# Kernel optimization log

Measured on AMD Instinct MI355X. Metric: run time of the kernel, lower is better.

## Reference

```python
import jax, jax.numpy as jnp
import numpy as np
import itertools

B, T, C, H = 2, 512, 768, 12
HS = C // H                      # head size 64
M = 8                            # dpp_top_m
MIN_SIZE, MAX_SIZE = 2, 3        # subset sizes including token i
TEMP = 1.0                       # dpp_temperature
ALPHA = 1.0                      # dpp_penalty_alpha
SIGN = 1.0                       # minimize_det=False -> +log_det
NEG = -1e30

# Static combination tables over the M top-k candidate slots, lexicographic order.
# Filtering combos that touch i's slot (or padding slots) reproduces
# itertools.combinations(topidx_list) order exactly.
COMBS = [np.array(list(itertools.combinations(range(M), s)), dtype=np.int32)
         for s in range(MIN_SIZE - 1, MAX_SIZE)]  # extra sizes 1 and 2


def _token(i, q_i, k, v):
    Tn = k.shape[0]
    sim = k @ q_i                                   # [T]
    sim = jnp.where(jnp.arange(Tn) <= i, sim, -jnp.inf)  # causal
    _, top_idx = jax.lax.top_k(sim, M)              # [M]
    n_cand = jnp.minimum(M, i + 1)
    slot_valid = jnp.arange(M) < n_cand             # padding slots invalid
    slot_is_i = (top_idx == i) & slot_valid
    scores, outs, valids = [], [], []
    for comb in COMBS:
        slots = jnp.asarray(comb)                   # [nc, s]
        nc, s = comb.shape
        valid = slot_valid[slots].all(axis=1) & (~slot_is_i[slots].any(axis=1))
        idx = jnp.concatenate(
            [jnp.full((nc, 1), i, dtype=top_idx.dtype), top_idx[slots]], axis=1)  # [nc, s+1]
        K = k[idx]                                  # [nc, s+1, hs]
        V = v[idx]
        gram = jnp.einsum('cnd,cmd->cnm', K, K)     # [nc, s+1, s+1]
        det = jnp.linalg.det(gram)
        log_det = jnp.log(jnp.where(valid, det, 1.0) + 1e-6)
        score = SIGN * log_det / float(s + 1) ** ALPHA
        dot = jnp.einsum('cnd,d->cn', K, q_i) / HS ** 0.5
        w = jax.nn.softmax(dot, axis=1)
        out_s = jnp.einsum('cn,cnd->cd', w, V)      # [nc, hs]
        scores.append(jnp.where(valid, score, NEG))
        outs.append(out_s)
        valids.append(valid)
    scores = jnp.concatenate(scores)                # [36]
    outs = jnp.concatenate(outs, axis=0)            # [36, hs]
    has_valid = jnp.concatenate(valids).any()
    probs = jax.nn.softmax(scores / TEMP)
    best = jnp.argmax(probs)
    y_st = outs[best]
    y_soft = probs @ outs
    # straight-through: forward value = y_soft, gradient flows through y_st
    y = y_st + jax.lax.stop_gradient(y_soft - y_st)
    return jnp.where(has_valid, y, v[i])


def _dpp_head(q, k, v):  # q,k,v: [T, hs]
    return jax.vmap(lambda i, qi: _token(i, qi, k, v))(jnp.arange(q.shape[0]), q)


def _forward(x, W_attn, b_attn, W_proj, b_proj):
    Bx, Tx, Cx = x.shape
    qkv = x @ W_attn.T + b_attn                     # [B, T, 3C]
    q, k, v = jnp.split(qkv, 3, axis=2)

    def heads(t):  # [B, T, C] -> [B*H, T, hs]
        return t.reshape(Bx, Tx, H, HS).transpose(0, 2, 1, 3).reshape(Bx * H, Tx, HS)

    y = jax.vmap(_dpp_head)(heads(q), heads(k), heads(v))  # [B*H, T, hs]
    y = y.reshape(Bx, H, Tx, HS).transpose(0, 2, 1, 3).reshape(Bx, Tx, Cx)
    return y @ W_proj.T + b_proj


def setup_inputs() -> dict:
    key = jax.random.key(0)
    k1, k2, k3, k4, k5 = jax.random.split(key, 5)
    return {
        'x': jax.random.normal(k1, (B, T, C), dtype=jnp.float32),
        'W_attn': jax.random.normal(k2, (3 * C, C), dtype=jnp.float32) * 0.02,
        'b_attn': jax.random.normal(k3, (3 * C,), dtype=jnp.float32) * 0.02,
        'W_proj': jax.random.normal(k4, (C, C), dtype=jnp.float32) * 0.02,
        'b_proj': jax.random.normal(k5, (C,), dtype=jnp.float32) * 0.02,
    }


def reference(x, W_attn, b_attn, W_proj, b_proj):
    return _forward(x, W_attn, b_attn, W_proj, b_proj)
```

## Files before the change

kernel.cpp:

```cpp
#include <hip/hip_runtime.h>
#include <math.h>

#define Bn 2
#define Hn 12
#define Tn 512
#define Cn 768
#define HS 64
#define BH 24
#define MTOP 8
#define NCOMB 36
#define NEGV -1e30f

#define NX (Bn * Tn * Cn)
#define NW (3 * Cn * Cn)
#define NP (Cn * Cn)

typedef __bf16 bf16x8 __attribute__((ext_vector_type(8)));
typedef float f32x4 __attribute__((ext_vector_type(4)));

__device__ __constant__ int C_SL0[NCOMB] = {
  0,1,2,3,4,5,6,7,
  0,0,0,0,0,0,0,
  1,1,1,1,1,1,
  2,2,2,2,2,
  3,3,3,3,
  4,4,4,
  5,5,
  6};
__device__ __constant__ int C_SL1[NCOMB] = {
  -1,-1,-1,-1,-1,-1,-1,-1,
  1,2,3,4,5,6,7,
  2,3,4,5,6,7,
  3,4,5,6,7,
  4,5,6,7,
  5,6,7,
  6,7,
  7};

__device__ __constant__ int PA[45] = {
  0,0,0,0,0,0,0,0,0,
  1,1,1,1,1,1,1,1,
  2,2,2,2,2,2,2,
  3,3,3,3,3,3,
  4,4,4,4,4,
  5,5,5,5,
  6,6,6,
  7,7,
  8};
__device__ __constant__ int PB[45] = {
  0,1,2,3,4,5,6,7,8,
  1,2,3,4,5,6,7,8,
  2,3,4,5,6,7,8,
  3,4,5,6,7,8,
  4,5,6,7,8,
  5,6,7,8,
  6,7,8,
  7,8,
  8};

__device__ __constant__ int TI[36] = {
  0,1,1,2,2,2,3,3,3,3,4,4,4,4,4,5,5,5,5,5,5,6,6,6,6,6,6,6,7,7,7,7,7,7,7,7};
__device__ __constant__ int TJ[36] = {
  0,0,1,0,1,2,0,1,2,3,0,1,2,3,4,0,1,2,3,4,5,0,1,2,3,4,5,6,0,1,2,3,4,5,6,7};

__device__ __forceinline__ unsigned short bf_rne(float x) {
    unsigned u = __float_as_uint(x);
    return (unsigned short)((u + 0x7fff + ((u >> 16) & 1)) >> 16);
}
__device__ __forceinline__ float bf_f(unsigned short s) {
    return __uint_as_float(((unsigned)s) << 16);
}

template<int CTRL, int RM>
__device__ __forceinline__ float dpp_add_step(float x) {
    int t = __builtin_amdgcn_update_dpp(0, __float_as_int(x), CTRL, RM, 0xf, false);
    return x + __int_as_float(t);
}
template<int CTRL, int RM>
__device__ __forceinline__ float dpp_max_step(float x) {
    int t = __builtin_amdgcn_update_dpp((int)0xFF800000, __float_as_int(x), CTRL, RM, 0xf, false);
    return fmaxf(x, __int_as_float(t));
}
__device__ __forceinline__ float wave_sum(float x) {
    x = dpp_add_step<0x111, 0xf>(x);
    x = dpp_add_step<0x112, 0xf>(x);
    x = dpp_add_step<0x114, 0xf>(x);
    x = dpp_add_step<0x118, 0xf>(x);
    x = dpp_add_step<0x142, 0xa>(x);
    x = dpp_add_step<0x143, 0xc>(x);
    return __int_as_float(__builtin_amdgcn_readlane(__float_as_int(x), 63));
}
__device__ __forceinline__ float wave_max(float x) {
    x = dpp_max_step<0x111, 0xf>(x);
    x = dpp_max_step<0x112, 0xf>(x);
    x = dpp_max_step<0x114, 0xf>(x);
    x = dpp_max_step<0x118, 0xf>(x);
    x = dpp_max_step<0x142, 0xa>(x);
    x = dpp_max_step<0x143, 0xc>(x);
    return __int_as_float(__builtin_amdgcn_readlane(__float_as_int(x), 63));
}

__global__ __launch_bounds__(256) void conv_all(const float* __restrict__ x,
                                                const float* __restrict__ Wa,
                                                const float* __restrict__ Wp,
                                                unsigned short* __restrict__ xcat,
                                                unsigned short* __restrict__ Wcat,
                                                unsigned short* __restrict__ Wpbf) {
    int idx = blockIdx.x * 256 + threadIdx.x;
    if (idx < NX) {
        int r = idx / Cn, c = idx - r * Cn;
        float v = x[idx];
        unsigned short h = bf_rne(v);
        unsigned short l = bf_rne(v - bf_f(h));
        size_t base = (size_t)r * 2304 + c;
        xcat[base] = h;
        xcat[base + 768] = h;
        xcat[base + 1536] = l;
    } else if (idx < NX + NW) {
        int j = idx - NX;
        int r = j / Cn, c = j - r * Cn;
        float v = Wa[j];
        unsigned short h = bf_rne(v);
        unsigned short l = bf_rne(v - bf_f(h));
        size_t base = (size_t)r * 2304 + c;
        Wcat[base] = h;
        Wcat[base + 1536] = h;
        Wcat[base + 768] = l;
    } else if (idx < NX + NW + NP) {
        int j = idx - NX - NW;
        Wpbf[j] = bf_rne(Wp[j]);
    }
}

__device__ __forceinline__ void gemm_core(const unsigned short* __restrict__ Ag,
                                          const unsigned short* __restrict__ Bg,
                                          int Kst, int NS,
                                          unsigned short* Ab, unsigned short* Bb,
                                          f32x4 acc[2][2]) {
    const int tid = threadIdx.x;
    const int wv = tid >> 6, lane = tid & 63;
    const int r0 = tid >> 3;
    const int c8 = (tid & 7) * 8;
    const int m0w = (wv >> 1) * 32;
    const int n0w = (wv & 1) * 32;
    const int fr = lane & 15;
    const int fk = (lane >> 4) * 8;

    const unsigned short* pa0 = Ag + (size_t)r0 * Kst + c8;
    const unsigned short* pa1 = Ag + (size_t)(r0 + 32) * Kst + c8;
    const unsigned short* pb0 = Bg + (size_t)r0 * Kst + c8;
    const unsigned short* pb1 = Bg + (size_t)(r0 + 32) * Kst + c8;

    bf16x8 raA0 = *(const bf16x8*)pa0;
    bf16x8 raA1 = *(const bf16x8*)pa1;
    bf16x8 rbA0 = *(const bf16x8*)pb0;
    bf16x8 rbA1 = *(const bf16x8*)pb1;
    bf16x8 raB0 = *(const bf16x8*)(pa0 + 64);
    bf16x8 raB1 = *(const bf16x8*)(pa1 + 64);
    bf16x8 rbB0 = *(const bf16x8*)(pb0 + 64);
    bf16x8 rbB1 = *(const bf16x8*)(pb1 + 64);

    const int sO = r0 * 72 + c8;

    auto compute = [&](int bufo) {
        #pragma unroll
        for (int ks = 0; ks < 2; ++ks) {
            bf16x8 af[2], bg[2];
            #pragma unroll
            for (int mi = 0; mi < 2; ++mi)
                af[mi] = *(const bf16x8*)(Ab + bufo + (m0w + 16 * mi + fr) * 72 + ks * 32 + fk);
            #pragma unroll
            for (int ni = 0; ni < 2; ++ni)
                bg[ni] = *(const bf16x8*)(Bb + bufo + (n0w + 16 * ni + fr) * 72 + ks * 32 + fk);
            #pragma unroll
            for (int mi = 0; mi < 2; ++mi)
                #pragma unroll
                for (int ni = 0; ni < 2; ++ni)
                    acc[mi][ni] = __builtin_amdgcn_mfma_f32_16x16x32_bf16(af[mi], bg[ni], acc[mi][ni], 0, 0, 0);
        }
    };

    for (int s = 0; s < NS; s += 2) {
        *(bf16x8*)(Ab + sO)           = raA0;
        *(bf16x8*)(Ab + sO + 32 * 72) = raA1;
        *(bf16x8*)(Bb + sO)           = rbA0;
        *(bf16x8*)(Bb + sO + 32 * 72) = rbA1;
        __syncthreads();
        if (s + 2 < NS) {
            raA0 = *(const bf16x8*)(pa0 + (s + 2) * 64);
            raA1 = *(const bf16x8*)(pa1 + (s + 2) * 64);
            rbA0 = *(const bf16x8*)(pb0 + (s + 2) * 64);
            rbA1 = *(const bf16x8*)(pb1 + (s + 2) * 64);
        }
        compute(0);

        *(bf16x8*)(Ab + 4608 + sO)           = raB0;
        *(bf16x8*)(Ab + 4608 + sO + 32 * 72) = raB1;
        *(bf16x8*)(Bb + 4608 + sO)           = rbB0;
        *(bf16x8*)(Bb + 4608 + sO + 32 * 72) = rbB1;
        __syncthreads();
        if (s + 3 < NS) {
            raB0 = *(const bf16x8*)(pa0 + (s + 3) * 64);
            raB1 = *(const bf16x8*)(pa1 + (s + 3) * 64);
            rbB0 = *(const bf16x8*)(pb0 + (s + 3) * 64);
            rbB1 = *(const bf16x8*)(pb1 + (s + 3) * 64);
        }
        compute(4608);
    }
}

__global__ __launch_bounds__(256) void mfma_qkv(const unsigned short* __restrict__ xcat,
                                                const unsigned short* __restrict__ Wcat,
                                                const float* __restrict__ bias,
                                                unsigned short* __restrict__ qcat,
                                                unsigned short* __restrict__ kcat,
                                                float* __restrict__ vh) {
    __shared__ unsigned short Ab[2 * 64 * 72];
    __shared__ unsigned short Bb[2 * 64 * 72];
    const int tm = blockIdx.x * 64;
    const int by = blockIdx.y;
    const int wv = threadIdx.x >> 6, lane = threadIdx.x & 63;
    const int kq = lane >> 4, r = lane & 15;
    f32x4 acc[2][2] = {};

    if (by < 24) {
        const int tn = by * 64;
        gemm_core(xcat + (size_t)tm * 2304, Wcat + (size_t)tn * 2304, 2304, 36, Ab, Bb, acc);
        const int part = tn / Cn;
        #pragma unroll
        for (int mi = 0; mi < 2; ++mi) {
            #pragma unroll
            for (int ni = 0; ni < 2; ++ni) {
                #pragma unroll
                for (int rr = 0; rr < 4; ++rr) {
                    int mm = tm + (wv >> 1) * 32 + mi * 16 + kq * 4 + rr;
                    int nn = tn + (wv & 1) * 32 + ni * 16 + r;
                    float val = acc[mi][ni][rr] + bias[nn];
                    int bb = mm >> 9, t = mm & 511;
                    int c = nn - part * Cn;
                    int h = c >> 6, d = c & 63;
                    int bh = bb * Hn + h;
                    unsigned short s1 = bf_rne(val);
                    float r1 = val - bf_f(s1);
                    unsigned short s2 = bf_rne(r1);
                    unsigned short s3 = bf_rne(r1 - bf_f(s2));
                    size_t base = ((size_t)bh * Tn + t) * 384 + d;
                    if (part == 0) {
                        qcat[base]       = s1;
                        qcat[base + 64]  = s1;
                        qcat[base + 192] = s1;
                        qcat[base + 128] = s2;
                        qcat[base + 320] = s2;
                        qcat[base + 256] = s3;
                    } else {
                        kcat[base]       = s1;
                        kcat[base + 128] = s1;
                        kcat[base + 256] = s1;
                        kcat[base + 64]  = s2;
                        kcat[base + 320] = s2;
                        kcat[base + 192] = s3;
                    }
                }
            }
        }
    } else {
        const int hvi = by - 24;
        const int cv = hvi * 64;
        gemm_core(xcat + (size_t)tm * 2304,
                  Wcat + (size_t)(1536 + cv) * 2304, 2304, 12, Ab, Bb, acc);
        #pragma unroll
        for (int mi = 0; mi < 2; ++mi) {
            #pragma unroll
            for (int ni = 0; ni < 2; ++ni) {
                #pragma unroll
                for (int rr = 0; rr < 4; ++rr) {
                    int mm = tm + (wv >> 1) * 32 + mi * 16 + kq * 4 + rr;
                    int nloc = (wv & 1) * 32 + ni * 16 + r;
                    float val = acc[mi][ni][rr] + bias[1536 + cv + nloc];
                    int bb = mm >> 9, t = mm & 511;
                    int bh = bb * Hn + hvi;
                    vh[((size_t)bh * Tn + t) * HS + nloc] = val;
                }
            }
        }
    }
}

__global__ __launch_bounds__(256) void mfma_sim(const unsigned short* __restrict__ qcat,
                                                const unsigned short* __restrict__ kcat,
                                                float* __restrict__ S) {
    __shared__ unsigned short Ab[2 * 64 * 72];
    __shared__ unsigned short Bb[2 * 64 * 72];
    const int bh = blockIdx.y;
    const int ti = TI[blockIdx.x], tj = TJ[blockIdx.x];
    f32x4 acc[2][2] = {};
    gemm_core(qcat + ((size_t)bh * Tn + ti * 64) * 384,
              kcat + ((size_t)bh * Tn + tj * 64) * 384, 384, 6, Ab, Bb, acc);

    const int wv = threadIdx.x >> 6, lane = threadIdx.x & 63;
    const int kq = lane >> 4, r = lane & 15;
    float* Sp = S + (size_t)bh * 147456 + (size_t)(ti * (ti + 1) / 2 + tj) * 4096;
    #pragma unroll
    for (int mi = 0; mi < 2; ++mi)
        #pragma unroll
        for (int ni = 0; ni < 2; ++ni)
            #pragma unroll
            for (int rr = 0; rr < 4; ++rr) {
                int ml = (wv >> 1) * 32 + mi * 16 + kq * 4 + rr;
                int nl = (wv & 1) * 32 + ni * 16 + r;
                Sp[ml * 64 + nl] = acc[mi][ni][rr];
            }
}

__global__ __launch_bounds__(256) void mfma_proj(const unsigned short* __restrict__ Abf,
                                                 const unsigned short* __restrict__ Bbf,
                                                 const float* __restrict__ bias,
                                                 float* __restrict__ outp) {
    __shared__ unsigned short Ab[2 * 64 * 72];
    __shared__ unsigned short Bb[2 * 64 * 72];
    const int tm = blockIdx.x * 64;
    const int tn = blockIdx.y * 64;
    f32x4 acc[2][2] = {};
    gemm_core(Abf + (size_t)tm * Cn, Bbf + (size_t)tn * Cn, Cn, 12, Ab, Bb, acc);

    const int wv = threadIdx.x >> 6, lane = threadIdx.x & 63;
    const int kq = lane >> 4, r = lane & 15;
    #pragma unroll
    for (int mi = 0; mi < 2; ++mi)
        #pragma unroll
        for (int ni = 0; ni < 2; ++ni)
            #pragma unroll
            for (int rr = 0; rr < 4; ++rr) {
                int mm = tm + (wv >> 1) * 32 + mi * 16 + kq * 4 + rr;
                int nn = tn + (wv & 1) * 32 + ni * 16 + r;
                outp[(size_t)mm * Cn + nn] = acc[mi][ni][rr] + bias[nn];
            }
}

#define CEF(arr, ia, ib) { \
    float _a = arr[ia], _b = arr[ib]; \
    arr[ia] = fmaxf(_a, _b); arr[ib] = fminf(_a, _b); }

__global__ __launch_bounds__(256) void dpp_kernel(const float* __restrict__ S,
                                                  const unsigned short* __restrict__ kcat,
                                                  const float* __restrict__ vh,
                                                  unsigned short* __restrict__ yb) {
    const int bh = blockIdx.x;
    const int w = threadIdx.x >> 6;
    const int lane = threadIdx.x & 63;
    const int ibase = blockIdx.y * 8 + w * 2;

    __shared__ float KshW[8][9][68];
    __shared__ float VshW[8][9][65];
    __shared__ float Gsh[8][81];
    __shared__ float qdsh[8][12];
    const float* Sbh = S + (size_t)bh * 147456;
    const unsigned short* kc = kcat + (size_t)bh * Tn * 384;
    const float* vbase = vh + (size_t)bh * Tn * HS;

    int ii[2], tib[2];
    float sv[2][8];
    float qd0[2];
    #pragma unroll
    for (int tt = 0; tt < 2; ++tt) {
        const int i = ibase + tt;
        ii[tt] = i;
        const int t8 = i >> 6;
        tib[tt] = t8;
        const int tribase = t8 * (t8 + 1) / 2;
        const int rloc = (i & 63) * 64;
        #pragma unroll
        for (int rr = 0; rr < 8; ++rr) {
            sv[tt][rr] = -INFINITY;
            if (rr <= t8) {
                int j = rr * 64 + lane;
                float s = Sbh[(size_t)(tribase + rr) * 4096 + rloc + lane];
                sv[tt][rr] = (j <= i) ? s : -INFINITY;
            }
        }
        qd0[tt] = Sbh[(size_t)(tribase + t8) * 4096 + rloc + (i & 63)];
    }

    float key[2][8];
    #pragma unroll
    for (int tt = 0; tt < 2; ++tt)
        #pragma unroll
        for (int r = 0; r < 8; ++r) key[tt][r] = sv[tt][r];

    #pragma unroll
    for (int tt = 0; tt < 2; ++tt) {
        CEF(key[tt],0,1) CEF(key[tt],2,3) CEF(key[tt],4,5) CEF(key[tt],6,7)
        CEF(key[tt],0,2) CEF(key[tt],1,3) CEF(key[tt],4,6) CEF(key[tt],5,7)
        CEF(key[tt],1,2) CEF(key[tt],5,6)
        CEF(key[tt],0,4) CEF(key[tt],1,5) CEF(key[tt],2,6) CEF(key[tt],3,7)
        CEF(key[tt],2,4) CEF(key[tt],3,5)
        CEF(key[tt],1,2) CEF(key[tt],3,4) CEF(key[tt],5,6)
    }

    #pragma unroll
    for (int st = 0; st < 6; ++st) {
        const int off = 1 << st;
        #pragma unroll
        for (int tt = 0; tt < 2; ++tt) {
            float pk[8];
            #pragma unroll
            for (int r = 0; r < 8; ++r)
                pk[r] = __shfl_xor(key[tt][r], off, 64);
            float t[8];
            #pragma unroll
            for (int r = 0; r < 8; ++r)
                t[r] = fmaxf(key[tt][r], pk[7 - r]);
            CEF(t,0,4) CEF(t,1,5) CEF(t,2,6) CEF(t,3,7)
            CEF(t,0,2) CEF(t,1,3) CEF(t,4,6) CEF(t,5,7)
            CEF(t,0,1) CEF(t,2,3) CEF(t,4,5) CEF(t,6,7)
            #pragma unroll
            for (int r = 0; r < 8; ++r) key[tt][r] = t[r];
        }
    }

    int topi[2][8];
    float topv[2][8];
    #pragma unroll
    for (int tt = 0; tt < 2; ++tt) {
        unsigned long long used[8] = {0, 0, 0, 0, 0, 0, 0, 0};
        #pragma unroll
        for (int p = 0; p < 8; ++p) {
            float v = key[tt][p];
            topv[tt][p] = v;
            int idx = ii[tt];
            bool found = false;
            #pragma unroll
            for (int r = 0; r < 8; ++r) {
                unsigned long long m = __ballot(sv[tt][r] == v) & ~used[r];
                if (!found && m != 0ull) {
                    int l = __builtin_ctzll(m);
                    idx = r * 64 + l;
                    used[r] |= (1ull << l);
                    found = true;
                }
            }
            topi[tt][p] = idx;
        }
    }

    #pragma unroll
    for (int tt = 0; tt < 2; ++tt) {
        const int ctx = w * 2 + tt;
        #pragma unroll
        for (int a = 0; a < 9; ++a) {
            int t = (a == 0) ? ii[tt] : topi[tt][a - 1];
            size_t kb = (size_t)t * 384 + lane;
            KshW[ctx][a][lane] = bf_f(kc[kb]) + bf_f(kc[kb + 64]) + bf_f(kc[kb + 192]);
            VshW[ctx][a][lane] = vbase[(size_t)t * HS + lane];
        }
        if (lane < 9) {
            float val = qd0[tt];
            #pragma unroll
            for (int p = 0; p < 8; ++p) if (lane == p + 1) val = topv[tt][p];
            qdsh[ctx][lane] = val;
        }
    }

    if (lane < 45) {
        const int a = PA[lane], b = PB[lane];
        #pragma unroll
        for (int tt = 0; tt < 2; ++tt) {
            const int ctx = w * 2 + tt;
            const float4* rka = (const float4*)&KshW[ctx][a][0];
            const float4* rkb = (const float4*)&KshW[ctx][b][0];
            float acc = 0.f;
            #pragma unroll
            for (int t = 0; t < 16; ++t) {
                float4 fa = rka[t], fb = rkb[t];
                acc += fa.x * fb.x; acc += fa.y * fb.y;
                acc += fa.z * fb.z; acc += fa.w * fb.w;
            }
            Gsh[ctx][a * 9 + b] = acc;
            Gsh[ctx][b * 9 + a] = acc;
        }
    }

    const int sl0c = (lane < NCOMB) ? C_SL0[lane] : -1;
    const int sl1c = (lane < NCOMB) ? C_SL1[lane] : -1;
    float score[2]; int ca[2], cb[2], sdim[2];
    #pragma unroll
    for (int tt = 0; tt < 2; ++tt) {
        const int ctx = w * 2 + tt;
        const int i = ii[tt];
        const int n_cand = (i + 1 < MTOP) ? (i + 1) : MTOP;
        int vmask = 0;
        #pragma unroll
        for (int s = 0; s < MTOP; ++s)
            if (s < n_cand && topi[tt][s] != i) vmask |= (1 << s);

        score[tt] = -INFINITY; ca[tt] = 0; cb[tt] = 0; sdim[tt] = 1;
        if (lane < NCOMB) {
            sdim[tt] = (sl1c < 0) ? 1 : 2;
            ca[tt] = sl0c + 1;
            cb[tt] = (sl1c < 0) ? 0 : sl1c + 1;
            bool valid = ((vmask >> sl0c) & 1);
            if (sdim[tt] == 2) valid = valid && ((vmask >> sl1c) & 1);
            float G00 = Gsh[ctx][0];
            float Gaa = Gsh[ctx][ca[tt] * 9 + ca[tt]];
            float G0a = Gsh[ctx][ca[tt]];
            float det;
            if (sdim[tt] == 1) {
                det = G00 * Gaa - G0a * G0a;
            } else {
                float G0b = Gsh[ctx][cb[tt]];
                float Gab = Gsh[ctx][ca[tt] * 9 + cb[tt]];
                float Gbb = Gsh[ctx][cb[tt] * 9 + cb[tt]];
                det = G00 * (Gaa * Gbb - Gab * Gab)
                    - G0a * (G0a * Gbb - Gab * G0b)
                    + G0b * (G0a * Gab - Gaa * G0b);
            }
            score[tt] = valid ? (logf(det + 1e-6f) / (float)(sdim[tt] + 1)) : NEGV;
        }
    }

    float mxv[2], sumv[2], ee[2];
    #pragma unroll
    for (int tt = 0; tt < 2; ++tt) mxv[tt] = wave_max(score[tt]);
    #pragma unroll
    for (int tt = 0; tt < 2; ++tt)
        ee[tt] = (lane < NCOMB) ? expf(score[tt] - mxv[tt]) : 0.f;
    #pragma unroll
    for (int tt = 0; tt < 2; ++tt) sumv[tt] = wave_sum(ee[tt]);

    float pwx[2] = {0.f, 0.f}, pwy[2] = {0.f, 0.f}, pwz[2] = {0.f, 0.f};
    #pragma unroll
    for (int tt = 0; tt < 2; ++tt) {
        const int ctx = w * 2 + tt;
        if (lane < NCOMB) {
            float prob = ee[tt] / sumv[tt];
            float d0 = qdsh[ctx][0]      * 0.125f;
            float d1 = qdsh[ctx][ca[tt]] * 0.125f;
            float d2 = (sdim[tt] == 2) ? qdsh[ctx][cb[tt]] * 0.125f : -INFINITY;
            float m2 = fmaxf(fmaxf(d0, d1), d2);
            float e0 = expf(d0 - m2), e1 = expf(d1 - m2);
            float e2 = (sdim[tt] == 2) ? expf(d2 - m2) : 0.f;
            float inv = prob / (e0 + e1 + e2);
            pwx[tt] = e0 * inv; pwy[tt] = e1 * inv; pwz[tt] = e2 * inv;
        }
    }

    float c0[2], cs[2][8];
    #pragma unroll
    for (int tt = 0; tt < 2; ++tt) {
        c0[tt] = wave_sum(pwx[tt]);
        #pragma unroll
        for (int s = 0; s < 8; ++s) {
            float contrib = ((sl0c == s) ? pwy[tt] : 0.f) + ((sl1c == s) ? pwz[tt] : 0.f);
            cs[tt][s] = wave_sum(contrib);
        }
    }

    #pragma unroll
    for (int tt = 0; tt < 2; ++tt) {
        const int ctx = w * 2 + tt;
        const bool hasValid = (mxv[tt] > -1e29f);
        const float v0 = VshW[ctx][0][lane];
        float y = v0;
        if (hasValid) {
            y = c0[tt] * v0;
            #pragma unroll
            for (int s = 0; s < 8; ++s)
                y += cs[tt][s] * VshW[ctx][s + 1][lane];
        }
        const int bb = bh / Hn, h = bh % Hn;
        yb[((size_t)(bb * Tn + ii[tt])) * Cn + h * HS + lane] = bf_rne(y);
    }
}

extern "C" void kernel_launch(void* const* d_in, const int* in_sizes, int n_in,
                              void* d_out, int out_size, void* d_ws, size_t ws_size,
                              hipStream_t stream) {
    const float* x      = (const float*)d_in[0];
    const float* W_attn = (const float*)d_in[1];
    const float* b_attn = (const float*)d_in[2];
    const float* W_proj = (const float*)d_in[3];
    const float* b_proj = (const float*)d_in[4];
    float* out = (float*)d_out;

    char* ws = (char*)d_ws;
    float* vh            = (float*)(ws);
    unsigned short* qcat = (unsigned short*)(ws + 3145728);
    unsigned short* kcat = (unsigned short*)(ws + 12582912);
    unsigned short* xcat = (unsigned short*)(ws + 22020096);
    unsigned short* Wcat = (unsigned short*)(ws + 26738688);
    float* S             = (float*)(ws + 26738688);
    unsigned short* ybf  = xcat;
    unsigned short* Wpbf = (unsigned short*)(ws + 40894464);

    conv_all<<<dim3((NX + NW + NP + 255) / 256), 256, 0, stream>>>(
        x, W_attn, W_proj, xcat, Wcat, Wpbf);

    mfma_qkv<<<dim3(16, 36), 256, 0, stream>>>(xcat, Wcat, b_attn, qcat, kcat, vh);

    mfma_sim<<<dim3(36, BH), 256, 0, stream>>>(qcat, kcat, S);

    dpp_kernel<<<dim3(BH, Tn / 8), 256, 0, stream>>>(S, kcat, vh, ybf);

    mfma_proj<<<dim3(16, 12), 256, 0, stream>>>(ybf, Wpbf, b_proj, out);
}
```

Baseline: 152.1 us.

## Use direct global-to-LDS loads with triple-buffered XOR-swizzled tiles in GEMM core

Replaces the register-staged double-buffered GEMM tile loading with global_load_lds direct-to-LDS transfers into three rotating buffers, waiting with vmcnt and a raw s_barrier. The padded 72-stride layout becomes an XOR-swizzled 64-stride layout to avoid bank conflicts without padding. The aim is to drop the register round trip and one barrier per step, and to keep two tiles in flight. It relies on the exact LDS placement behaviour of global_load_lds per wave and on manual waitcnt correctness. The change may give wrong results if the loop has a write-after-read hazard on the reused buffer.

```diff
diff --git a/kernel.cpp b/kernel.cpp
--- a/kernel.cpp
+++ b/kernel.cpp
@@ -132,46 +132,62 @@
     }
 }
 
+__device__ __forceinline__ void gld16(const unsigned short* g, unsigned short* l) {
+    __builtin_amdgcn_global_load_lds(
+        (const __attribute__((address_space(1))) unsigned short*)g,
+        (__attribute__((address_space(3))) unsigned short*)l, 16, 0, 0);
+}
+
 __device__ __forceinline__ void gemm_core(const unsigned short* __restrict__ Ag,
                                           const unsigned short* __restrict__ Bg,
                                           int Kst, int NS,
-                                          unsigned short* Ab, unsigned short* Bb,
+                                          unsigned short* LB,
                                           f32x4 acc[2][2]) {
     const int tid = threadIdx.x;
     const int wv = tid >> 6, lane = tid & 63;
     const int r0 = tid >> 3;
-    const int c8 = (tid & 7) * 8;
+    const int sg = tid & 7;
+    const int gsg = sg ^ (r0 & 7);
     const int m0w = (wv >> 1) * 32;
     const int n0w = (wv & 1) * 32;
     const int fr = lane & 15;
-    const int fk = (lane >> 4) * 8;
-
-    const unsigned short* pa0 = Ag + (size_t)r0 * Kst + c8;
-    const unsigned short* pa1 = Ag + (size_t)(r0 + 32) * Kst + c8;
-    const unsigned short* pb0 = Bg + (size_t)r0 * Kst + c8;
-    const unsigned short* pb1 = Bg + (size_t)(r0 + 32) * Kst + c8;
-
-    bf16x8 raA0 = *(const bf16x8*)pa0;
-    bf16x8 raA1 = *(const bf16x8*)pa1;
-    bf16x8 rbA0 = *(const bf16x8*)pb0;
-    bf16x8 rbA1 = *(const bf16x8*)pb1;
-    bf16x8 raB0 = *(const bf16x8*)(pa0 + 64);
-    bf16x8 raB1 = *(const bf16x8*)(pa1 + 64);
-    bf16x8 rbB0 = *(const bf16x8*)(pb0 + 64);
-    bf16x8 rbB1 = *(const bf16x8*)(pb1 + 64);
-
-    const int sO = r0 * 72 + c8;
-
-    auto compute = [&](int bufo) {
+    const int tq = lane >> 4;
+
+    const unsigned short* pa0 = Ag + (size_t)r0 * Kst + gsg * 8;
+    const unsigned short* pa1 = Ag + (size_t)(r0 + 32) * Kst + gsg * 8;
+    const unsigned short* pb0 = Bg + (size_t)r0 * Kst + gsg * 8;
+    const unsigned short* pb1 = Bg + (size_t)(r0 + 32) * Kst + gsg * 8;
+
+    unsigned short* lA = LB + wv * 512;
+    unsigned short* lB = LB + 4096 + wv * 512;
+
+    auto issue = [&](int s, int b) {
+        const int cb = s * 64;
+        unsigned short* a  = lA + b * 8192;
+        unsigned short* bb = lB + b * 8192;
+        gld16(pa0 + cb, a);
+        gld16(pa1 + cb, a + 2048);
+        gld16(pb0 + cb, bb);
+        gld16(pb1 + cb, bb + 2048);
+    };
+
+    auto compute = [&](int b) {
+        const unsigned short* Ab = LB + b * 8192;
+        const unsigned short* Bb = Ab + 4096;
         #pragma unroll
         for (int ks = 0; ks < 2; ++ks) {
+            const int t = ks * 4 + tq;
             bf16x8 af[2], bg[2];
             #pragma unroll
-            for (int mi = 0; mi < 2; ++mi)
-                af[mi] = *(const bf16x8*)(Ab + bufo + (m0w + 16 * mi + fr) * 72 + ks * 32 + fk);
-            #pragma unroll
-            for (int ni = 0; ni < 2; ++ni)
-                bg[ni] = *(const bf16x8*)(Bb + bufo + (n0w + 16 * ni + fr) * 72 + ks * 32 + fk);
+            for (int mi = 0; mi < 2; ++mi) {
+                const int row = m0w + 16 * mi + fr;
+                af[mi] = *(const bf16x8*)(Ab + row * 64 + (t ^ (row & 7)) * 8);
+            }
+            #pragma unroll
+            for (int ni = 0; ni < 2; ++ni) {
+                const int row = n0w + 16 * ni + fr;
+                bg[ni] = *(const bf16x8*)(Bb + row * 64 + (t ^ (row & 7)) * 8);
+            }
             #pragma unroll
             for (int mi = 0; mi < 2; ++mi)
                 #pragma unroll
@@ -180,32 +196,19 @@
         }
     };
 
-    for (int s = 0; s < NS; s += 2) {
-        *(bf16x8*)(Ab + sO)           = raA0;
-        *(bf16x8*)(Ab + sO + 32 * 72) = raA1;
-        *(bf16x8*)(Bb + sO)           = rbA0;
-        *(bf16x8*)(Bb + sO + 32 * 72) = rbA1;
-        __syncthreads();
+    issue(0, 0);
+    issue(1, 1);
+    int b = 0;
+    for (int s = 0; s < NS; ++s) {
+        if (s + 1 < NS) asm volatile("s_waitcnt vmcnt(4)" ::: "memory");
+        else            asm volatile("s_waitcnt vmcnt(0)" ::: "memory");
+        __builtin_amdgcn_s_barrier();
         if (s + 2 < NS) {
-            raA0 = *(const bf16x8*)(pa0 + (s + 2) * 64);
-            raA1 = *(const bf16x8*)(pa1 + (s + 2) * 64);
-            rbA0 = *(const bf16x8*)(pb0 + (s + 2) * 64);
-            rbA1 = *(const bf16x8*)(pb1 + (s + 2) * 64);
-        }
-        compute(0);
-
-        *(bf16x8*)(Ab + 4608 + sO)           = raB0;
-        *(bf16x8*)(Ab + 4608 + sO + 32 * 72) = raB1;
-        *(bf16x8*)(Bb + 4608 + sO)           = rbB0;
-        *(bf16x8*)(Bb + 4608 + sO + 32 * 72) = rbB1;
-        __syncthreads();
-        if (s + 3 < NS) {
-            raB0 = *(const bf16x8*)(pa0 + (s + 3) * 64);
-            raB1 = *(const bf16x8*)(pa1 + (s + 3) * 64);
-            rbB0 = *(const bf16x8*)(pb0 + (s + 3) * 64);
-            rbB1 = *(const bf16x8*)(pb1 + (s + 3) * 64);
-        }
-        compute(4608);
+            int bn = b + 2; if (bn >= 3) bn -= 3;
+            issue(s + 2, bn);
+        }
+        compute(b);
+        if (++b == 3) b = 0;
     }
 }
 
@@ -215,8 +218,7 @@
                                                 unsigned short* __restrict__ qcat,
                                                 unsigned short* __restrict__ kcat,
                                                 float* __restrict__ vh) {
-    __shared__ unsigned short Ab[2 * 64 * 72];
-    __shared__ unsigned short Bb[2 * 64 * 72];
+    __shared__ __align__(16) unsigned short LB[3 * 8192];
     const int tm = blockIdx.x * 64;
     const int by = blockIdx.y;
     const int wv = threadIdx.x >> 6, lane = threadIdx.x & 63;
@@ -225,7 +227,7 @@
 
     if (by < 24) {
         const int tn = by * 64;
-        gemm_core(xcat + (size_t)tm * 2304, Wcat + (size_t)tn * 2304, 2304, 36, Ab, Bb, acc);
+        gemm_core(xcat + (size_t)tm * 2304, Wcat + (size_t)tn * 2304, 2304, 36, LB, acc);
         const int part = tn / Cn;
         #pragma unroll
         for (int mi = 0; mi < 2; ++mi) {
@@ -267,7 +269,7 @@
         const int hvi = by - 24;
         const int cv = hvi * 64;
         gemm_core(xcat + (size_t)tm * 2304,
-                  Wcat + (size_t)(1536 + cv) * 2304, 2304, 12, Ab, Bb, acc);
+                  Wcat + (size_t)(1536 + cv) * 2304, 2304, 12, LB, acc);
         #pragma unroll
         for (int mi = 0; mi < 2; ++mi) {
             #pragma unroll
@@ -289,13 +291,12 @@
 __global__ __launch_bounds__(256) void mfma_sim(const unsigned short* __restrict__ qcat,
                                                 const unsigned short* __restrict__ kcat,
                                                 float* __restrict__ S) {
-    __shared__ unsigned short Ab[2 * 64 * 72];
-    __shared__ unsigned short Bb[2 * 64 * 72];
+    __shared__ __align__(16) unsigned short LB[3 * 8192];
     const int bh = blockIdx.y;
     const int ti = TI[blockIdx.x], tj = TJ[blockIdx.x];
     f32x4 acc[2][2] = {};
     gemm_core(qcat + ((size_t)bh * Tn + ti * 64) * 384,
-              kcat + ((size_t)bh * Tn + tj * 64) * 384, 384, 6, Ab, Bb, acc);
+              kcat + ((size_t)bh * Tn + tj * 64) * 384, 384, 6, LB, acc);
 
     const int wv = threadIdx.x >> 6, lane = threadIdx.x & 63;
     const int kq = lane >> 4, r = lane & 15;
@@ -316,12 +317,11 @@
                                                  const unsigned short* __restrict__ Bbf,
                                                  const float* __restrict__ bias,
                                                  float* __restrict__ outp) {
-    __shared__ unsigned short Ab[2 * 64 * 72];
-    __shared__ unsigned short Bb[2 * 64 * 72];
+    __shared__ __align__(16) unsigned short LB[3 * 8192];
     const int tm = blockIdx.x * 64;
     const int tn = blockIdx.y * 64;
     f32x4 acc[2][2] = {};
-    gemm_core(Abf + (size_t)tm * Cn, Bbf + (size_t)tn * Cn, Cn, 12, Ab, Bb, acc);
+    gemm_core(Abf + (size_t)tm * Cn, Bbf + (size_t)tn * Cn, Cn, 12, LB, acc);
 
     const int wv = threadIdx.x >> 6, lane = threadIdx.x & 63;
     const int kq = lane >> 4, r = lane & 15;
```

After: 148.4 us. 1.02x faster.
